# Kernel optimization log

Measured on AMD Instinct MI355X. Metric: run time of the kernel, lower is better.

Reference implementation:

```python
import jax, jax.numpy as jnp
import numpy as np

N_NODES = 100000
N_EDGES = 1600000
N_GRAPHS = 512
NODE_DIM = 64   # len(node_indices)
GRAPH_DIM = 16  # len(graph_indices) == graph_channels
HIDDEN = 128
OUT = 8


def setup_inputs() -> dict:
    key = jax.random.key(0)
    ks = jax.random.split(key, 12)
    x = jax.random.normal(ks[0], (N_NODES, NODE_DIM + GRAPH_DIM), dtype=jnp.float32)
    edge_index = jax.random.randint(ks[1], (2, N_EDGES), 0, N_NODES, dtype=jnp.int64)
    batch = jnp.sort(jax.random.randint(ks[2], (N_NODES,), 0, N_GRAPHS, dtype=jnp.int64))
    def lin(k, fan_in, fan_out):
        lim = 1.0 / np.sqrt(fan_in)
        return jax.random.uniform(k, (fan_in, fan_out), jnp.float32, -lim, lim)
    return {
        "x": x, "edge_index": edge_index, "batch": batch,
        "W1": lin(ks[3], NODE_DIM, HIDDEN), "b1": jnp.zeros((HIDDEN,), jnp.float32),
        "W2": lin(ks[4], HIDDEN, HIDDEN),   "b2": jnp.zeros((HIDDEN,), jnp.float32),
        "Wm1": lin(ks[5], HIDDEN + GRAPH_DIM, HIDDEN), "bm1": jnp.zeros((HIDDEN,), jnp.float32),
        "Wm2": lin(ks[6], HIDDEN, OUT), "bm2": jnp.zeros((OUT,), jnp.float32),
    }


def _gcn_conv(h_in, src, dst, W, b):
    # PyG GCNConv: h = X W; out = D^{-1/2}(A+I)D^{-1/2} h + b, deg over A+I.
    h = h_in @ W                                        # [N, H]
    deg = jnp.zeros((N_NODES,), h.dtype).at[dst].add(1.0) + 1.0  # +1 self loop
    dinv = jax.lax.rsqrt(deg)                           # [N]
    norm = dinv[src] * dinv[dst]                        # [E]
    out = jnp.zeros_like(h).at[dst].add(norm[:, None] * h[src])
    out = out + (dinv * dinv)[:, None] * h              # self-loop term
    return out + b


def _mean_pool(v, batch):
    cnt = jax.ops.segment_sum(jnp.ones((v.shape[0],), v.dtype), batch, num_segments=N_GRAPHS)
    s = jax.ops.segment_sum(v, batch, num_segments=N_GRAPHS)
    return s / jnp.maximum(cnt, 1.0)[:, None]


def reference(x, edge_index, batch, W1, b1, W2, b2, Wm1, bm1, Wm2, bm2):
    src, dst = edge_index[0], edge_index[1]
    node_t = x[:, :NODE_DIM]                 # node_indices slice
    graph_t = _mean_pool(x[:, NODE_DIM:], batch)  # graph_indices slice, pooled [G, 16]
    h = _gcn_conv(node_t, src, dst, W1, b1)
    h = jax.nn.relu(h)                       # dropout is identity in eval mode
    h = _gcn_conv(h, src, dst, W2, b2)
    g = _mean_pool(h, batch)                 # [G, H]
    g = jnp.concatenate([g, graph_t], axis=1)
    g = jax.nn.relu(g @ Wm1 + bm1)
    return g @ Wm2 + bm2                     # [G, OUT]
```

## Files before the change

kernel.cpp:

```cpp
#include <hip/hip_runtime.h>
#include <hip/hip_bf16.h>

#define N_NODES 100000
#define N_EDGES 1600000
#define N_GRAPHS 512
#define NODE_DIM 64
#define GRAPH_DIM 16
#define HIDDEN 128
#define OUT_DIM 8

#define NBUCKETS 391
#define BIN_CAP 8192
#define EPB 4096


__global__ __launch_bounds__(256) void k_binplace(const int* __restrict__ src,
                                                  const int* __restrict__ dst,
                                                  int* __restrict__ gcur,
                                                  unsigned* __restrict__ bin) {
    __shared__ int cnt[NBUCKETS];
    __shared__ int base[NBUCKETS];
    int t = threadIdx.x;
    for (int i = t; i < NBUCKETS; i += 256) cnt[i] = 0;
    __syncthreads();
    int e0 = blockIdx.x * EPB;
#pragma unroll
    for (int k = 0; k < EPB / 256; k++) {
        int e = e0 + k * 256 + t;
        if (e < N_EDGES) atomicAdd(&cnt[dst[e] >> 8], 1);
    }
    __syncthreads();
    for (int i = t; i < NBUCKETS; i += 256) {
        int c = cnt[i];
        base[i] = (c > 0) ? atomicAdd(&gcur[i], c) : 0;
        cnt[i] = 0;
    }
    __syncthreads();
#pragma unroll
    for (int k = 0; k < EPB / 256; k++) {
        int e = e0 + k * 256 + t;
        if (e < N_EDGES) {
            int d = dst[e];
            int b = d >> 8;
            int p = atomicAdd(&cnt[b], 1);
            bin[(size_t)b * BIN_CAP + base[b] + p] = ((unsigned)src[e] << 8) | (unsigned)(d & 255);
        }
    }
}


__global__ __launch_bounds__(256) void k_degBf(const int* __restrict__ gcur,
                                               const unsigned* __restrict__ bin,
                                               int* __restrict__ degcnt,
                                               float* __restrict__ dinv,
                                               int* __restrict__ bsum) {
    __shared__ int cnt[256];
    int b = blockIdx.x, t = threadIdx.x;
    cnt[t] = 0;
    __syncthreads();
    int n = gcur[b];
    const unsigned* seg = bin + (size_t)b * BIN_CAP;
    for (int i = t; i < n; i += 256) atomicAdd(&cnt[seg[i] & 255u], 1);
    __syncthreads();
    int c = cnt[t];
    int node = b * 256 + t;
    if (node < N_NODES) {
        degcnt[node] = c;
        dinv[node] = rsqrtf((float)c + 1.0f);
    }
    __syncthreads();
    for (int o = 128; o > 0; o >>= 1) {
        if (t < o) cnt[t] += cnt[t + o];
        __syncthreads();
    }
    if (t == 0) bsum[b] = cnt[0];
}


__global__ __launch_bounds__(512) void k_scanb(const int* __restrict__ bsum,
                                               int* __restrict__ bofs) {
    __shared__ int s[512];
    int t = threadIdx.x;
    int v = (t < NBUCKETS) ? bsum[t] : 0;
    s[t] = v;
    __syncthreads();
    for (int o = 1; o < 512; o <<= 1) {
        int u = (t >= o) ? s[t - o] : 0;
        __syncthreads();
        s[t] += u;
        __syncthreads();
    }
    if (t < NBUCKETS) bofs[t] = s[t] - v;
}


__global__ __launch_bounds__(256) void k_rowfill(const int* __restrict__ degcnt,
                                                 const int* __restrict__ bofs,
                                                 const int* __restrict__ gcur,
                                                 const unsigned* __restrict__ bin,
                                                 const float* __restrict__ dinv,
                                                 int* __restrict__ row_start,
                                                 int* __restrict__ csr,
                                                 float* __restrict__ csrw) {
    __shared__ int sc[256];
    __shared__ int rsl[256];
    __shared__ int cnt[256];
    __shared__ float dl[256];
    int b = blockIdx.x, t = threadIdx.x;
    int node = b * 256 + t;
    int v = (node < N_NODES) ? degcnt[node] : 0;
    sc[t] = v;
    __syncthreads();
    for (int o = 1; o < 256; o <<= 1) {
        int u = (t >= o) ? sc[t - o] : 0;
        __syncthreads();
        sc[t] += u;
        __syncthreads();
    }
    int rs = bofs[b] + sc[t] - v;
    if (node < N_NODES) row_start[node] = rs;
    rsl[t] = rs;
    cnt[t] = 0;
    dl[t] = rsqrtf((float)v + 1.0f);
    __syncthreads();
    int n = gcur[b];
    const unsigned* seg = bin + (size_t)b * BIN_CAP;
    for (int i = t; i < n; i += 256) {
        unsigned e = seg[i];
        int dlidx = (int)(e & 255u);
        int s = (int)(e >> 8);
        int pos = rsl[dlidx] + atomicAdd(&cnt[dlidx], 1);
        csr[pos] = s;
        csrw[pos] = dinv[s] * dl[dlidx];
    }
}


__global__ __launch_bounds__(256) void k_packstat(const float* __restrict__ x,
                                                  const int* __restrict__ batch,
                                                  ushort* __restrict__ xb,
                                                  float* __restrict__ gt_sum) {
    int t = threadIdx.x;
    int i0 = blockIdx.x * 64;
    for (int idx = t; idx < 64 * 32; idx += 256) {
        int node = i0 + (idx >> 5);
        if (node < N_NODES) {
            int c2 = idx & 31;
            float2 v = *(const float2*)&x[(size_t)node * 80 + c2 * 2];
            __hip_bfloat16 lo = __float2bfloat16(v.x);
            __hip_bfloat16 hi = __float2bfloat16(v.y);
            ushort2 pv = make_ushort2(*(ushort*)&lo, *(ushort*)&hi);
            ((ushort2*)xb)[(size_t)node * 32 + c2] = pv;
        }
    }
    int c = t & 15, sub = t >> 4;
    int iend = min(i0 + 64, N_NODES);
    float acc = 0.0f;
    int g = -1;
    for (int i = i0 + sub; i < iend; i += 16) {
        int bi = batch[i];
        if (bi != g) {
            if (g >= 0) atomicAdd(&gt_sum[g * GRAPH_DIM + c], acc);
            acc = 0.0f; g = bi;
        }
        acc += x[(size_t)i * 80 + NODE_DIM + c];
    }
    if (g >= 0) atomicAdd(&gt_sum[g * GRAPH_DIM + c], acc);
}


#define LDX(s_) __uint_as_float((unsigned)xb[(size_t)(s_)*64 + lane] << 16)

__global__ __launch_bounds__(256) void k_gather1(const int* __restrict__ csr,
                                                 const float* __restrict__ csrw,
                                                 const int* __restrict__ row_start,
                                                 const float* __restrict__ dinv,
                                                 const ushort* __restrict__ xb,
                                                 float* __restrict__ z) {
    int w = threadIdx.x >> 6, lane = threadIdx.x & 63;
    int nA = blockIdx.x * 8 + w * 2;
    int nB = nA + 1;
    int rsA = row_start[nA], reA = (nA == N_NODES - 1) ? N_EDGES : row_start[nA + 1];
    int rsB = row_start[nB], reB = (nB == N_NODES - 1) ? N_EDGES : row_start[nB + 1];
    float aA0 = 0.f, aA1 = 0.f, aA2 = 0.f, aA3 = 0.f;
    float aB0 = 0.f, aB1 = 0.f, aB2 = 0.f, aB3 = 0.f;
    int kA = rsA, kB = rsB;
    while (kA + 4 <= reA && kB + 4 <= reB) {
        int a0 = csr[kA], a1 = csr[kA + 1], a2 = csr[kA + 2], a3 = csr[kA + 3];
        int b0 = csr[kB], b1 = csr[kB + 1], b2 = csr[kB + 2], b3 = csr[kB + 3];
        float wa0 = csrw[kA], wa1 = csrw[kA + 1], wa2 = csrw[kA + 2], wa3 = csrw[kA + 3];
        float wb0 = csrw[kB], wb1 = csrw[kB + 1], wb2 = csrw[kB + 2], wb3 = csrw[kB + 3];
        float vA0 = LDX(a0), vA1 = LDX(a1), vA2 = LDX(a2), vA3 = LDX(a3);
        float vB0 = LDX(b0), vB1 = LDX(b1), vB2 = LDX(b2), vB3 = LDX(b3);
        aA0 += wa0 * vA0; aA1 += wa1 * vA1; aA2 += wa2 * vA2; aA3 += wa3 * vA3;
        aB0 += wb0 * vB0; aB1 += wb1 * vB1; aB2 += wb2 * vB2; aB3 += wb3 * vB3;
        kA += 4; kB += 4;
    }
    while (kA + 4 <= reA) {
        int a0 = csr[kA], a1 = csr[kA + 1], a2 = csr[kA + 2], a3 = csr[kA + 3];
        float wa0 = csrw[kA], wa1 = csrw[kA + 1], wa2 = csrw[kA + 2], wa3 = csrw[kA + 3];
        float vA0 = LDX(a0), vA1 = LDX(a1), vA2 = LDX(a2), vA3 = LDX(a3);
        aA0 += wa0 * vA0; aA1 += wa1 * vA1; aA2 += wa2 * vA2; aA3 += wa3 * vA3;
        kA += 4;
    }
    while (kB + 4 <= reB) {
        int b0 = csr[kB], b1 = csr[kB + 1], b2 = csr[kB + 2], b3 = csr[kB + 3];
        float wb0 = csrw[kB], wb1 = csrw[kB + 1], wb2 = csrw[kB + 2], wb3 = csrw[kB + 3];
        float vB0 = LDX(b0), vB1 = LDX(b1), vB2 = LDX(b2), vB3 = LDX(b3);
        aB0 += wb0 * vB0; aB1 += wb1 * vB1; aB2 += wb2 * vB2; aB3 += wb3 * vB3;
        kB += 4;
    }
    while (kA < reA && kB < reB) {
        int a0 = csr[kA]; int b0 = csr[kB];
        float wa0 = csrw[kA], wb0 = csrw[kB];
        aA0 += wa0 * LDX(a0); aB0 += wb0 * LDX(b0);
        kA++; kB++;
    }
    while (kA < reA) { int a0 = csr[kA]; aA0 += csrw[kA] * LDX(a0); kA++; }
    while (kB < reB) { int b0 = csr[kB]; aB0 += csrw[kB] * LDX(b0); kB++; }
    float dA = dinv[nA], dB = dinv[nB];
    z[(size_t)nA * 64 + lane] = aA0 + aA1 + aA2 + aA3 + dA * dA * LDX(nA);
    z[(size_t)nB * 64 + lane] = aB0 + aB1 + aB2 + aB3 + dB * dB * LDX(nB);
}


__global__ __launch_bounds__(128) void k_gemm64(const float* __restrict__ A,
                                                const float* __restrict__ W,
                                                const float* __restrict__ bias,
                                                ushort* __restrict__ C, int nrows) {
    const int TM = 8, K = 64;
    __shared__ float As[TM][K];
    int row0 = blockIdx.x * TM;
    int j = threadIdx.x;
    for (int idx = threadIdx.x; idx < TM * K; idx += 128) {
        int m = idx / K, k = idx % K;
        int r = row0 + m;
        As[m][k] = (r < nrows) ? A[(size_t)r * K + k] : 0.0f;
    }
    __syncthreads();
    float acc[TM];
#pragma unroll
    for (int m = 0; m < TM; m++) acc[m] = 0.0f;
    for (int k = 0; k < K; k++) {
        float w = W[k * 128 + j];
#pragma unroll
        for (int m = 0; m < TM; m++) acc[m] += As[m][k] * w;
    }
    float b = bias[j];
#pragma unroll
    for (int m = 0; m < TM; m++) {
        int r = row0 + m;
        if (r < nrows) {
            float v = fmaxf(acc[m] + b, 0.0f);
            __hip_bfloat16 hv = __float2bfloat16(v);
            C[(size_t)r * 128 + j] = *(ushort*)&hv;
        }
    }
}


__global__ __launch_bounds__(256) void k_gather2(const int* __restrict__ csr,
                                                 const float* __restrict__ csrw,
                                                 const int* __restrict__ row_start,
                                                 const float* __restrict__ dinv,
                                                 const unsigned* __restrict__ h,
                                                 const int* __restrict__ batch,
                                                 float* __restrict__ gsum2) {
    __shared__ float2 red[8][64];
    int w = threadIdx.x >> 6, lane = threadIdx.x & 63;
    int nA = blockIdx.x * 8 + w * 2;
    int nB = nA + 1;
    int rsA = row_start[nA], reA = (nA == N_NODES - 1) ? N_EDGES : row_start[nA + 1];
    int rsB = row_start[nB], reB = (nB == N_NODES - 1) ? N_EDGES : row_start[nB + 1];
    float2 aA0 = {0.f,0.f}, aA1 = {0.f,0.f}, aA2 = {0.f,0.f}, aA3 = {0.f,0.f};
    float2 aB0 = {0.f,0.f}, aB1 = {0.f,0.f}, aB2 = {0.f,0.f}, aB3 = {0.f,0.f};
    int kA = rsA, kB = rsB;
#define FMA2(acc_, w_, u_) { acc_.x += (w_) * __uint_as_float((u_) << 16); \
                             acc_.y += (w_) * __uint_as_float((u_) & 0xffff0000u); }
    while (kA + 4 <= reA && kB + 4 <= reB) {
        int a0 = csr[kA], a1 = csr[kA + 1], a2 = csr[kA + 2], a3 = csr[kA + 3];
        int b0 = csr[kB], b1 = csr[kB + 1], b2 = csr[kB + 2], b3 = csr[kB + 3];
        float wa0 = csrw[kA], wa1 = csrw[kA + 1], wa2 = csrw[kA + 2], wa3 = csrw[kA + 3];
        float wb0 = csrw[kB], wb1 = csrw[kB + 1], wb2 = csrw[kB + 2], wb3 = csrw[kB + 3];
        unsigned uA0 = h[(size_t)a0 * 64 + lane], uA1 = h[(size_t)a1 * 64 + lane];
        unsigned uA2 = h[(size_t)a2 * 64 + lane], uA3 = h[(size_t)a3 * 64 + lane];
        unsigned uB0 = h[(size_t)b0 * 64 + lane], uB1 = h[(size_t)b1 * 64 + lane];
        unsigned uB2 = h[(size_t)b2 * 64 + lane], uB3 = h[(size_t)b3 * 64 + lane];
        FMA2(aA0, wa0, uA0); FMA2(aA1, wa1, uA1); FMA2(aA2, wa2, uA2); FMA2(aA3, wa3, uA3);
        FMA2(aB0, wb0, uB0); FMA2(aB1, wb1, uB1); FMA2(aB2, wb2, uB2); FMA2(aB3, wb3, uB3);
        kA += 4; kB += 4;
    }
    while (kA + 4 <= reA) {
        int a0 = csr[kA], a1 = csr[kA + 1], a2 = csr[kA + 2], a3 = csr[kA + 3];
        float wa0 = csrw[kA], wa1 = csrw[kA + 1], wa2 = csrw[kA + 2], wa3 = csrw[kA + 3];
        unsigned uA0 = h[(size_t)a0 * 64 + lane], uA1 = h[(size_t)a1 * 64 + lane];
        unsigned uA2 = h[(size_t)a2 * 64 + lane], uA3 = h[(size_t)a3 * 64 + lane];
        FMA2(aA0, wa0, uA0); FMA2(aA1, wa1, uA1); FMA2(aA2, wa2, uA2); FMA2(aA3, wa3, uA3);
        kA += 4;
    }
    while (kB + 4 <= reB) {
        int b0 = csr[kB], b1 = csr[kB + 1], b2 = csr[kB + 2], b3 = csr[kB + 3];
        float wb0 = csrw[kB], wb1 = csrw[kB + 1], wb2 = csrw[kB + 2], wb3 = csrw[kB + 3];
        unsigned uB0 = h[(size_t)b0 * 64 + lane], uB1 = h[(size_t)b1 * 64 + lane];
        unsigned uB2 = h[(size_t)b2 * 64 + lane], uB3 = h[(size_t)b3 * 64 + lane];
        FMA2(aB0, wb0, uB0); FMA2(aB1, wb1, uB1); FMA2(aB2, wb2, uB2); FMA2(aB3, wb3, uB3);
        kB += 4;
    }
    while (kA < reA && kB < reB) {
        int a0 = csr[kA]; int b0 = csr[kB];
        float wa0 = csrw[kA], wb0 = csrw[kB];
        unsigned uA0 = h[(size_t)a0 * 64 + lane], uB0 = h[(size_t)b0 * 64 + lane];
        FMA2(aA0, wa0, uA0); FMA2(aB0, wb0, uB0);
        kA++; kB++;
    }
    while (kA < reA) {
        int a0 = csr[kA]; float wa0 = csrw[kA];
        unsigned uA0 = h[(size_t)a0 * 64 + lane];
        FMA2(aA0, wa0, uA0); kA++;
    }
    while (kB < reB) {
        int b0 = csr[kB]; float wb0 = csrw[kB];
        unsigned uB0 = h[(size_t)b0 * 64 + lane];
        FMA2(aB0, wb0, uB0); kB++;
    }
    float dA = dinv[nA], dB = dinv[nB];
    unsigned usA = h[(size_t)nA * 64 + lane];
    unsigned usB = h[(size_t)nB * 64 + lane];
    float2 rA, rB;
    rA.x = aA0.x + aA1.x + aA2.x + aA3.x + dA * dA * __uint_as_float(usA << 16);
    rA.y = aA0.y + aA1.y + aA2.y + aA3.y + dA * dA * __uint_as_float(usA & 0xffff0000u);
    rB.x = aB0.x + aB1.x + aB2.x + aB3.x + dB * dB * __uint_as_float(usB << 16);
    rB.y = aB0.y + aB1.y + aB2.y + aB3.y + dB * dB * __uint_as_float(usB & 0xffff0000u);
    red[w * 2][lane] = rA;
    red[w * 2 + 1][lane] = rB;
    __syncthreads();
    int g0 = batch[blockIdx.x * 8];
    int g7 = batch[blockIdx.x * 8 + 7];
    if (g0 == g7) {
        if (w == 0) {
            float sx = 0.f, sy = 0.f;
#pragma unroll
            for (int q = 0; q < 8; q++) { sx += red[q][lane].x; sy += red[q][lane].y; }
            atomicAdd(&gsum2[g0 * 128 + 2 * lane], sx);
            atomicAdd(&gsum2[g0 * 128 + 2 * lane + 1], sy);
        }
    } else {
        int gA = batch[nA], gB = batch[nB];
        atomicAdd(&gsum2[gA * 128 + 2 * lane], rA.x);
        atomicAdd(&gsum2[gA * 128 + 2 * lane + 1], rA.y);
        atomicAdd(&gsum2[gB * 128 + 2 * lane], rB.x);
        atomicAdd(&gsum2[gB * 128 + 2 * lane + 1], rB.y);
    }
#undef FMA2
}


__global__ __launch_bounds__(128) void k_mlp(const float* __restrict__ gsum2,
                                             const float* __restrict__ gt_sum,
                                             const int* __restrict__ batch,
                                             const float* __restrict__ W2,
                                             const float* __restrict__ b2,
                                             const float* __restrict__ Wm1,
                                             const float* __restrict__ bm1,
                                             const float* __restrict__ Wm2,
                                             const float* __restrict__ bm2,
                                             float* __restrict__ out) {
    __shared__ float srow[HIDDEN];
    __shared__ float g144[HIDDEN + GRAPH_DIM];
    __shared__ float sm[HIDDEN];
    __shared__ int cnt_sh;
    int b = blockIdx.x;
    int j = threadIdx.x;
    float raw = gsum2[b * 128 + j];
    float gtraw = (j < GRAPH_DIM) ? gt_sum[b * GRAPH_DIM + j] : 0.0f;
    if (j == 0) {
        int lo = 0, hi = N_NODES;
        while (lo < hi) { int m = (lo + hi) >> 1; if (batch[m] < b) lo = m + 1; else hi = m; }
        int a = lo;
        lo = 0; hi = N_NODES;
        while (lo < hi) { int m = (lo + hi) >> 1; if (batch[m] < b + 1) lo = m + 1; else hi = m; }
        cnt_sh = lo - a;
    }
    __syncthreads();
    float inv = 1.0f / fmaxf((float)cnt_sh, 1.0f);
    srow[j] = raw * inv;
    if (j < GRAPH_DIM) g144[128 + j] = gtraw * inv;
    __syncthreads();
    float z = b2[j];
    for (int k = 0; k < 128; k++) z += srow[k] * W2[k * 128 + j];
    g144[j] = z;
    __syncthreads();
    float acc = bm1[j];
    for (int k = 0; k < HIDDEN + GRAPH_DIM; k++) acc += g144[k] * Wm1[k * 128 + j];
    sm[j] = fmaxf(acc, 0.0f);
    __syncthreads();
    if (j < OUT_DIM) {
        float o = bm2[j];
        for (int k = 0; k < 128; k++) o += sm[k] * Wm2[k * OUT_DIM + j];
        out[b * OUT_DIM + j] = o;
    }
}

extern "C" void kernel_launch(void* const* d_in, const int* in_sizes, int n_in,
                              void* d_out, int out_size, void* d_ws, size_t ws_size,
                              hipStream_t stream) {
    const float* x    = (const float*)d_in[0];
    const int*   edge = (const int*)d_in[1];
    const int*   src  = edge;
    const int*   dst  = edge + N_EDGES;
    const int*   batch= (const int*)d_in[2];
    const float* W1   = (const float*)d_in[3];
    const float* b1   = (const float*)d_in[4];
    const float* W2   = (const float*)d_in[5];
    const float* b2   = (const float*)d_in[6];
    const float* Wm1  = (const float*)d_in[7];
    const float* bm1  = (const float*)d_in[8];
    const float* Wm2  = (const float*)d_in[9];
    const float* bm2  = (const float*)d_in[10];
    float* out = (float*)d_out;

    char* ws = (char*)d_ws;
    char* p = ws;
    unsigned* bin   = (unsigned*)p;  p += (size_t)NBUCKETS * BIN_CAP * 4;
    float* A        = (float*)p;     p += (size_t)N_NODES * 64 * 4;
    ushort* h1b     = (ushort*)p;    p += (size_t)N_NODES * 128 * 2;
    ushort* xb      = (ushort*)p;    p += (size_t)N_NODES * 64 * 2;
    int*   csr      = (int*)p;       p += (size_t)N_EDGES * 4;
    float* csrw     = (float*)p;     p += (size_t)N_EDGES * 4;
    int*   degcnt   = (int*)p;       p += (size_t)NBUCKETS * 256 * 4;
    int*   row_start= (int*)p;       p += (size_t)N_NODES * 4;
    float* dinv     = (float*)p;     p += (size_t)N_NODES * 4;
    int*   gcur     = (int*)p;       p += (size_t)NBUCKETS * 4;
    int*   bsum     = (int*)p;       p += 512 * 4;
    int*   bofs     = (int*)p;       p += 512 * 4;
    float* gt_sum   = (float*)p;     p += (size_t)N_GRAPHS * GRAPH_DIM * 4;
    float* gsum2    = (float*)p;     p += (size_t)N_GRAPHS * 128 * 4;

    hipMemsetAsync(gcur,   0, (size_t)NBUCKETS * 4, stream);
    hipMemsetAsync(gt_sum, 0, (size_t)N_GRAPHS * GRAPH_DIM * 4, stream);
    hipMemsetAsync(gsum2,  0, (size_t)N_GRAPHS * 128 * 4, stream);

    k_binplace<<<(N_EDGES + EPB - 1) / EPB, 256, 0, stream>>>(src, dst, gcur, bin);
    k_degBf<<<NBUCKETS, 256, 0, stream>>>(gcur, bin, degcnt, dinv, bsum);
    k_scanb<<<1, 512, 0, stream>>>(bsum, bofs);
    k_rowfill<<<NBUCKETS, 256, 0, stream>>>(degcnt, bofs, gcur, bin, dinv, row_start, csr, csrw);

    k_packstat<<<(N_NODES + 63) / 64, 256, 0, stream>>>(x, batch, xb, gt_sum);

    k_gather1<<<N_NODES / 8, 256, 0, stream>>>(csr, csrw, row_start, dinv, xb, A);
    k_gemm64<<<(N_NODES + 7) / 8, 128, 0, stream>>>(A, W1, b1, h1b, N_NODES);

    k_gather2<<<N_NODES / 8, 256, 0, stream>>>(csr, csrw, row_start, dinv,
                                               (const unsigned*)h1b, batch, gsum2);

    k_mlp<<<N_GRAPHS, 128, 0, stream>>>(gsum2, gt_sum, batch, W2, b2, Wm1, bm1, Wm2, bm2, out);
}
```

Before: 267.9 us.

## Interleave CSR index/weight, use half-wave per node with wider loads, fold memsets

Packs CSR source index and edge weight into one int2 array so each edge needs a single 8-byte load instead of two 4-byte loads. The gather kernels now assign one 32-lane half-wave per node and read wider vectors (two bf16 per lane in gather1, four in gather2), replacing the paired two-node interleaved loops. The zeroing of gt_sum and gsum2 moves from memset calls into earlier kernels (rowfill and gemm64), which removes two launches. The cost is fewer independent node streams per wave, which reduces the memory-level parallelism available to hide gather latency.

```diff
diff --git a/kernel.cpp b/kernel.cpp
--- a/kernel.cpp
+++ b/kernel.cpp
@@ -12,6 +12,9 @@
 #define NBUCKETS 391
 #define BIN_CAP 8192
 #define EPB 4096
+
+__device__ __forceinline__ float bflo(unsigned u) { return __uint_as_float(u << 16); }
+__device__ __forceinline__ float bfhi(unsigned u) { return __uint_as_float(u & 0xffff0000u); }
 
 
 __global__ __launch_bounds__(256) void k_binplace(const int* __restrict__ src,
@@ -100,13 +103,14 @@
                                                  const unsigned* __restrict__ bin,
                                                  const float* __restrict__ dinv,
                                                  int* __restrict__ row_start,
-                                                 int* __restrict__ csr,
-                                                 float* __restrict__ csrw) {
+                                                 int2* __restrict__ csre,
+                                                 float* __restrict__ gt_sum) {
     __shared__ int sc[256];
     __shared__ int rsl[256];
     __shared__ int cnt[256];
     __shared__ float dl[256];
     int b = blockIdx.x, t = threadIdx.x;
+    if (b < 32) gt_sum[b * 256 + t] = 0.0f;
     int node = b * 256 + t;
     int v = (node < N_NODES) ? degcnt[node] : 0;
     sc[t] = v;
@@ -130,8 +134,7 @@
         int dlidx = (int)(e & 255u);
         int s = (int)(e >> 8);
         int pos = rsl[dlidx] + atomicAdd(&cnt[dlidx], 1);
-        csr[pos] = s;
-        csrw[pos] = dinv[s] * dl[dlidx];
+        csre[pos] = make_int2(s, __float_as_int(dinv[s] * dl[dlidx]));
     }
 }
 
@@ -169,67 +172,64 @@
 }
 
 
-#define LDX(s_) __uint_as_float((unsigned)xb[(size_t)(s_)*64 + lane] << 16)
-
-__global__ __launch_bounds__(256) void k_gather1(const int* __restrict__ csr,
-                                                 const float* __restrict__ csrw,
+__global__ __launch_bounds__(256) void k_gather1(const int2* __restrict__ csre,
                                                  const int* __restrict__ row_start,
                                                  const float* __restrict__ dinv,
-                                                 const ushort* __restrict__ xb,
-                                                 float* __restrict__ z) {
-    int w = threadIdx.x >> 6, lane = threadIdx.x & 63;
-    int nA = blockIdx.x * 8 + w * 2;
-    int nB = nA + 1;
-    int rsA = row_start[nA], reA = (nA == N_NODES - 1) ? N_EDGES : row_start[nA + 1];
-    int rsB = row_start[nB], reB = (nB == N_NODES - 1) ? N_EDGES : row_start[nB + 1];
-    float aA0 = 0.f, aA1 = 0.f, aA2 = 0.f, aA3 = 0.f;
-    float aB0 = 0.f, aB1 = 0.f, aB2 = 0.f, aB3 = 0.f;
-    int kA = rsA, kB = rsB;
-    while (kA + 4 <= reA && kB + 4 <= reB) {
-        int a0 = csr[kA], a1 = csr[kA + 1], a2 = csr[kA + 2], a3 = csr[kA + 3];
-        int b0 = csr[kB], b1 = csr[kB + 1], b2 = csr[kB + 2], b3 = csr[kB + 3];
-        float wa0 = csrw[kA], wa1 = csrw[kA + 1], wa2 = csrw[kA + 2], wa3 = csrw[kA + 3];
-        float wb0 = csrw[kB], wb1 = csrw[kB + 1], wb2 = csrw[kB + 2], wb3 = csrw[kB + 3];
-        float vA0 = LDX(a0), vA1 = LDX(a1), vA2 = LDX(a2), vA3 = LDX(a3);
-        float vB0 = LDX(b0), vB1 = LDX(b1), vB2 = LDX(b2), vB3 = LDX(b3);
-        aA0 += wa0 * vA0; aA1 += wa1 * vA1; aA2 += wa2 * vA2; aA3 += wa3 * vA3;
-        aB0 += wb0 * vB0; aB1 += wb1 * vB1; aB2 += wb2 * vB2; aB3 += wb3 * vB3;
-        kA += 4; kB += 4;
-    }
-    while (kA + 4 <= reA) {
-        int a0 = csr[kA], a1 = csr[kA + 1], a2 = csr[kA + 2], a3 = csr[kA + 3];
-        float wa0 = csrw[kA], wa1 = csrw[kA + 1], wa2 = csrw[kA + 2], wa3 = csrw[kA + 3];
-        float vA0 = LDX(a0), vA1 = LDX(a1), vA2 = LDX(a2), vA3 = LDX(a3);
-        aA0 += wa0 * vA0; aA1 += wa1 * vA1; aA2 += wa2 * vA2; aA3 += wa3 * vA3;
-        kA += 4;
-    }
-    while (kB + 4 <= reB) {
-        int b0 = csr[kB], b1 = csr[kB + 1], b2 = csr[kB + 2], b3 = csr[kB + 3];
-        float wb0 = csrw[kB], wb1 = csrw[kB + 1], wb2 = csrw[kB + 2], wb3 = csrw[kB + 3];
-        float vB0 = LDX(b0), vB1 = LDX(b1), vB2 = LDX(b2), vB3 = LDX(b3);
-        aB0 += wb0 * vB0; aB1 += wb1 * vB1; aB2 += wb2 * vB2; aB3 += wb3 * vB3;
-        kB += 4;
-    }
-    while (kA < reA && kB < reB) {
-        int a0 = csr[kA]; int b0 = csr[kB];
-        float wa0 = csrw[kA], wb0 = csrw[kB];
-        aA0 += wa0 * LDX(a0); aB0 += wb0 * LDX(b0);
-        kA++; kB++;
-    }
-    while (kA < reA) { int a0 = csr[kA]; aA0 += csrw[kA] * LDX(a0); kA++; }
-    while (kB < reB) { int b0 = csr[kB]; aB0 += csrw[kB] * LDX(b0); kB++; }
-    float dA = dinv[nA], dB = dinv[nB];
-    z[(size_t)nA * 64 + lane] = aA0 + aA1 + aA2 + aA3 + dA * dA * LDX(nA);
-    z[(size_t)nB * 64 + lane] = aB0 + aB1 + aB2 + aB3 + dB * dB * LDX(nB);
+                                                 const unsigned* __restrict__ xb32,
+                                                 float2* __restrict__ z2) {
+    int w = threadIdx.x >> 6;
+    int half = (threadIdx.x >> 5) & 1;
+    int l = threadIdx.x & 31;
+    int node = blockIdx.x * 8 + w * 2 + half;
+    int rs = row_start[node];
+    int re = (node == N_NODES - 1) ? N_EDGES : row_start[node + 1];
+    float2 a0 = {0.f, 0.f}, a1 = {0.f, 0.f}, a2 = {0.f, 0.f}, a3 = {0.f, 0.f};
+    int k = rs;
+    for (; k + 4 <= re; k += 4) {
+        int2 e0 = csre[k], e1 = csre[k + 1], e2 = csre[k + 2], e3 = csre[k + 3];
+        unsigned u0 = xb32[(size_t)e0.x * 32 + l];
+        unsigned u1 = xb32[(size_t)e1.x * 32 + l];
+        unsigned u2 = xb32[(size_t)e2.x * 32 + l];
+        unsigned u3 = xb32[(size_t)e3.x * 32 + l];
+        float w0 = __int_as_float(e0.y), w1 = __int_as_float(e1.y);
+        float w2 = __int_as_float(e2.y), w3 = __int_as_float(e3.y);
+        a0.x += w0 * bflo(u0); a0.y += w0 * bfhi(u0);
+        a1.x += w1 * bflo(u1); a1.y += w1 * bfhi(u1);
+        a2.x += w2 * bflo(u2); a2.y += w2 * bfhi(u2);
+        a3.x += w3 * bflo(u3); a3.y += w3 * bfhi(u3);
+    }
+    if (k + 2 <= re) {
+        int2 e0 = csre[k], e1 = csre[k + 1];
+        unsigned u0 = xb32[(size_t)e0.x * 32 + l];
+        unsigned u1 = xb32[(size_t)e1.x * 32 + l];
+        float w0 = __int_as_float(e0.y), w1 = __int_as_float(e1.y);
+        a0.x += w0 * bflo(u0); a0.y += w0 * bfhi(u0);
+        a1.x += w1 * bflo(u1); a1.y += w1 * bfhi(u1);
+        k += 2;
+    }
+    if (k < re) {
+        int2 e0 = csre[k];
+        unsigned u0 = xb32[(size_t)e0.x * 32 + l];
+        float w0 = __int_as_float(e0.y);
+        a0.x += w0 * bflo(u0); a0.y += w0 * bfhi(u0);
+    }
+    float d = dinv[node];
+    unsigned us = xb32[(size_t)node * 32 + l];
+    float2 r;
+    r.x = a0.x + a1.x + a2.x + a3.x + d * d * bflo(us);
+    r.y = a0.y + a1.y + a2.y + a3.y + d * d * bfhi(us);
+    z2[(size_t)node * 32 + l] = r;
 }
 
 
 __global__ __launch_bounds__(128) void k_gemm64(const float* __restrict__ A,
                                                 const float* __restrict__ W,
                                                 const float* __restrict__ bias,
-                                                ushort* __restrict__ C, int nrows) {
+                                                ushort* __restrict__ C, int nrows,
+                                                float* __restrict__ gsum2) {
     const int TM = 8, K = 64;
     __shared__ float As[TM][K];
+    if (blockIdx.x < 512) gsum2[blockIdx.x * 128 + threadIdx.x] = 0.0f;
     int row0 = blockIdx.x * TM;
     int j = threadIdx.x;
     for (int idx = threadIdx.x; idx < TM * K; idx += 128) {
@@ -259,99 +259,82 @@
 }
 
 
-__global__ __launch_bounds__(256) void k_gather2(const int* __restrict__ csr,
-                                                 const float* __restrict__ csrw,
+__global__ __launch_bounds__(256) void k_gather2(const int2* __restrict__ csre,
                                                  const int* __restrict__ row_start,
                                                  const float* __restrict__ dinv,
-                                                 const unsigned* __restrict__ h,
+                                                 const uint2* __restrict__ h2,
                                                  const int* __restrict__ batch,
                                                  float* __restrict__ gsum2) {
-    __shared__ float2 red[8][64];
-    int w = threadIdx.x >> 6, lane = threadIdx.x & 63;
-    int nA = blockIdx.x * 8 + w * 2;
-    int nB = nA + 1;
-    int rsA = row_start[nA], reA = (nA == N_NODES - 1) ? N_EDGES : row_start[nA + 1];
-    int rsB = row_start[nB], reB = (nB == N_NODES - 1) ? N_EDGES : row_start[nB + 1];
-    float2 aA0 = {0.f,0.f}, aA1 = {0.f,0.f}, aA2 = {0.f,0.f}, aA3 = {0.f,0.f};
-    float2 aB0 = {0.f,0.f}, aB1 = {0.f,0.f}, aB2 = {0.f,0.f}, aB3 = {0.f,0.f};
-    int kA = rsA, kB = rsB;
-#define FMA2(acc_, w_, u_) { acc_.x += (w_) * __uint_as_float((u_) << 16); \
-                             acc_.y += (w_) * __uint_as_float((u_) & 0xffff0000u); }
-    while (kA + 4 <= reA && kB + 4 <= reB) {
-        int a0 = csr[kA], a1 = csr[kA + 1], a2 = csr[kA + 2], a3 = csr[kA + 3];
-        int b0 = csr[kB], b1 = csr[kB + 1], b2 = csr[kB + 2], b3 = csr[kB + 3];
-        float wa0 = csrw[kA], wa1 = csrw[kA + 1], wa2 = csrw[kA + 2], wa3 = csrw[kA + 3];
-        float wb0 = csrw[kB], wb1 = csrw[kB + 1], wb2 = csrw[kB + 2], wb3 = csrw[kB + 3];
-        unsigned uA0 = h[(size_t)a0 * 64 + lane], uA1 = h[(size_t)a1 * 64 + lane];
-        unsigned uA2 = h[(size_t)a2 * 64 + lane], uA3 = h[(size_t)a3 * 64 + lane];
-        unsigned uB0 = h[(size_t)b0 * 64 + lane], uB1 = h[(size_t)b1 * 64 + lane];
-        unsigned uB2 = h[(size_t)b2 * 64 + lane], uB3 = h[(size_t)b3 * 64 + lane];
-        FMA2(aA0, wa0, uA0); FMA2(aA1, wa1, uA1); FMA2(aA2, wa2, uA2); FMA2(aA3, wa3, uA3);
-        FMA2(aB0, wb0, uB0); FMA2(aB1, wb1, uB1); FMA2(aB2, wb2, uB2); FMA2(aB3, wb3, uB3);
-        kA += 4; kB += 4;
-    }
-    while (kA + 4 <= reA) {
-        int a0 = csr[kA], a1 = csr[kA + 1], a2 = csr[kA + 2], a3 = csr[kA + 3];
-        float wa0 = csrw[kA], wa1 = csrw[kA + 1], wa2 = csrw[kA + 2], wa3 = csrw[kA + 3];
-        unsigned uA0 = h[(size_t)a0 * 64 + lane], uA1 = h[(size_t)a1 * 64 + lane];
-        unsigned uA2 = h[(size_t)a2 * 64 + lane], uA3 = h[(size_t)a3 * 64 + lane];
-        FMA2(aA0, wa0, uA0); FMA2(aA1, wa1, uA1); FMA2(aA2, wa2, uA2); FMA2(aA3, wa3, uA3);
-        kA += 4;
-    }
-    while (kB + 4 <= reB) {
-        int b0 = csr[kB], b1 = csr[kB + 1], b2 = csr[kB + 2], b3 = csr[kB + 3];
-        float wb0 = csrw[kB], wb1 = csrw[kB + 1], wb2 = csrw[kB + 2], wb3 = csrw[kB + 3];
-        unsigned uB0 = h[(size_t)b0 * 64 + lane], uB1 = h[(size_t)b1 * 64 + lane];
-        unsigned uB2 = h[(size_t)b2 * 64 + lane], uB3 = h[(size_t)b3 * 64 + lane];
-        FMA2(aB0, wb0, uB0); FMA2(aB1, wb1, uB1); FMA2(aB2, wb2, uB2); FMA2(aB3, wb3, uB3);
-        kB += 4;
-    }
-    while (kA < reA && kB < reB) {
-        int a0 = csr[kA]; int b0 = csr[kB];
-        float wa0 = csrw[kA], wb0 = csrw[kB];
-        unsigned uA0 = h[(size_t)a0 * 64 + lane], uB0 = h[(size_t)b0 * 64 + lane];
-        FMA2(aA0, wa0, uA0); FMA2(aB0, wb0, uB0);
-        kA++; kB++;
-    }
-    while (kA < reA) {
-        int a0 = csr[kA]; float wa0 = csrw[kA];
-        unsigned uA0 = h[(size_t)a0 * 64 + lane];
-        FMA2(aA0, wa0, uA0); kA++;
-    }
-    while (kB < reB) {
-        int b0 = csr[kB]; float wb0 = csrw[kB];
-        unsigned uB0 = h[(size_t)b0 * 64 + lane];
-        FMA2(aB0, wb0, uB0); kB++;
-    }
-    float dA = dinv[nA], dB = dinv[nB];
-    unsigned usA = h[(size_t)nA * 64 + lane];
-    unsigned usB = h[(size_t)nB * 64 + lane];
-    float2 rA, rB;
-    rA.x = aA0.x + aA1.x + aA2.x + aA3.x + dA * dA * __uint_as_float(usA << 16);
-    rA.y = aA0.y + aA1.y + aA2.y + aA3.y + dA * dA * __uint_as_float(usA & 0xffff0000u);
-    rB.x = aB0.x + aB1.x + aB2.x + aB3.x + dB * dB * __uint_as_float(usB << 16);
-    rB.y = aB0.y + aB1.y + aB2.y + aB3.y + dB * dB * __uint_as_float(usB & 0xffff0000u);
-    red[w * 2][lane] = rA;
-    red[w * 2 + 1][lane] = rB;
-    __syncthreads();
-    int g0 = batch[blockIdx.x * 8];
-    int g7 = batch[blockIdx.x * 8 + 7];
+    __shared__ float4 red[8][32];
+    int w = threadIdx.x >> 6;
+    int half = (threadIdx.x >> 5) & 1;
+    int l = threadIdx.x & 31;
+    int slot = w * 2 + half;
+    int node = blockIdx.x * 8 + slot;
+    int rs = row_start[node];
+    int re = (node == N_NODES - 1) ? N_EDGES : row_start[node + 1];
+    float4 a0 = {0,0,0,0}, a1 = {0,0,0,0}, a2 = {0,0,0,0}, a3 = {0,0,0,0};
+#define FMA4(acc_, w_, u_) { acc_.x += (w_) * bflo((u_).x); acc_.y += (w_) * bfhi((u_).x); \
+                             acc_.z += (w_) * bflo((u_).y); acc_.w += (w_) * bfhi((u_).y); }
+    int k = rs;
+    for (; k + 4 <= re; k += 4) {
+        int2 e0 = csre[k], e1 = csre[k + 1], e2 = csre[k + 2], e3 = csre[k + 3];
+        uint2 u0 = h2[(size_t)e0.x * 32 + l];
+        uint2 u1 = h2[(size_t)e1.x * 32 + l];
+        uint2 u2 = h2[(size_t)e2.x * 32 + l];
+        uint2 u3 = h2[(size_t)e3.x * 32 + l];
+        float w0 = __int_as_float(e0.y), w1 = __int_as_float(e1.y);
+        float w2 = __int_as_float(e2.y), w3 = __int_as_float(e3.y);
+        FMA4(a0, w0, u0); FMA4(a1, w1, u1); FMA4(a2, w2, u2); FMA4(a3, w3, u3);
+    }
+    if (k + 2 <= re) {
+        int2 e0 = csre[k], e1 = csre[k + 1];
+        uint2 u0 = h2[(size_t)e0.x * 32 + l];
+        uint2 u1 = h2[(size_t)e1.x * 32 + l];
+        float w0 = __int_as_float(e0.y), w1 = __int_as_float(e1.y);
+        FMA4(a0, w0, u0); FMA4(a1, w1, u1);
+        k += 2;
+    }
+    if (k < re) {
+        int2 e0 = csre[k];
+        uint2 u0 = h2[(size_t)e0.x * 32 + l];
+        float w0 = __int_as_float(e0.y);
+        FMA4(a0, w0, u0);
+    }
+#undef FMA4
+    float d = dinv[node];
+    float dd = d * d;
+    uint2 us = h2[(size_t)node * 32 + l];
+    float4 r;
+    r.x = a0.x + a1.x + a2.x + a3.x + dd * bflo(us.x);
+    r.y = a0.y + a1.y + a2.y + a3.y + dd * bfhi(us.x);
+    r.z = a0.z + a1.z + a2.z + a3.z + dd * bflo(us.y);
+    r.w = a0.w + a1.w + a2.w + a3.w + dd * bfhi(us.y);
+    red[slot][l] = r;
+    __syncthreads();
+    int base8 = blockIdx.x * 8;
+    int g0 = batch[base8];
+    int g7 = batch[base8 + 7];
     if (g0 == g7) {
-        if (w == 0) {
-            float sx = 0.f, sy = 0.f;
-#pragma unroll
-            for (int q = 0; q < 8; q++) { sx += red[q][lane].x; sy += red[q][lane].y; }
-            atomicAdd(&gsum2[g0 * 128 + 2 * lane], sx);
-            atomicAdd(&gsum2[g0 * 128 + 2 * lane + 1], sy);
+        if (threadIdx.x < 32) {
+            float4 s = {0,0,0,0};
+#pragma unroll
+            for (int q = 0; q < 8; q++) {
+                float4 v = red[q][threadIdx.x];
+                s.x += v.x; s.y += v.y; s.z += v.z; s.w += v.w;
+            }
+            atomicAdd(&gsum2[g0 * 128 + threadIdx.x * 4 + 0], s.x);
+            atomicAdd(&gsum2[g0 * 128 + threadIdx.x * 4 + 1], s.y);
+            atomicAdd(&gsum2[g0 * 128 + threadIdx.x * 4 + 2], s.z);
+            atomicAdd(&gsum2[g0 * 128 + threadIdx.x * 4 + 3], s.w);
         }
     } else {
-        int gA = batch[nA], gB = batch[nB];
-        atomicAdd(&gsum2[gA * 128 + 2 * lane], rA.x);
-        atomicAdd(&gsum2[gA * 128 + 2 * lane + 1], rA.y);
-        atomicAdd(&gsum2[gB * 128 + 2 * lane], rB.x);
-        atomicAdd(&gsum2[gB * 128 + 2 * lane + 1], rB.y);
-    }
-#undef FMA2
+        int g = batch[node];
+        atomicAdd(&gsum2[g * 128 + l * 4 + 0], r.x);
+        atomicAdd(&gsum2[g * 128 + l * 4 + 1], r.y);
+        atomicAdd(&gsum2[g * 128 + l * 4 + 2], r.z);
+        atomicAdd(&gsum2[g * 128 + l * 4 + 3], r.w);
+    }
 }
 
 
@@ -422,11 +405,10 @@
     char* ws = (char*)d_ws;
     char* p = ws;
     unsigned* bin   = (unsigned*)p;  p += (size_t)NBUCKETS * BIN_CAP * 4;
+    int2*  csre     = (int2*)p;      p += (size_t)N_EDGES * 8;
     float* A        = (float*)p;     p += (size_t)N_NODES * 64 * 4;
     ushort* h1b     = (ushort*)p;    p += (size_t)N_NODES * 128 * 2;
     ushort* xb      = (ushort*)p;    p += (size_t)N_NODES * 64 * 2;
-    int*   csr      = (int*)p;       p += (size_t)N_EDGES * 4;
-    float* csrw     = (float*)p;     p += (size_t)N_EDGES * 4;
     int*   degcnt   = (int*)p;       p += (size_t)NBUCKETS * 256 * 4;
     int*   row_start= (int*)p;       p += (size_t)N_NODES * 4;
     float* dinv     = (float*)p;     p += (size_t)N_NODES * 4;
@@ -436,22 +418,20 @@
     float* gt_sum   = (float*)p;     p += (size_t)N_GRAPHS * GRAPH_DIM * 4;
     float* gsum2    = (float*)p;     p += (size_t)N_GRAPHS * 128 * 4;
 
-    hipMemsetAsync(gcur,   0, (size_t)NBUCKETS * 4, stream);
-    hipMemsetAsync(gt_sum, 0, (size_t)N_GRAPHS * GRAPH_DIM * 4, stream);
-    hipMemsetAsync(gsum2,  0, (size_t)N_GRAPHS * 128 * 4, stream);
+    hipMemsetAsync(gcur, 0, (size_t)NBUCKETS * 4, stream);
 
     k_binplace<<<(N_EDGES + EPB - 1) / EPB, 256, 0, stream>>>(src, dst, gcur, bin);
     k_degBf<<<NBUCKETS, 256, 0, stream>>>(gcur, bin, degcnt, dinv, bsum);
     k_scanb<<<1, 512, 0, stream>>>(bsum, bofs);
-    k_rowfill<<<NBUCKETS, 256, 0, stream>>>(degcnt, bofs, gcur, bin, dinv, row_start, csr, csrw);
+    k_rowfill<<<NBUCKETS, 256, 0, stream>>>(degcnt, bofs, gcur, bin, dinv, row_start, csre, gt_sum);
 
     k_packstat<<<(N_NODES + 63) / 64, 256, 0, stream>>>(x, batch, xb, gt_sum);
 
-    k_gather1<<<N_NODES / 8, 256, 0, stream>>>(csr, csrw, row_start, dinv, xb, A);
-    k_gemm64<<<(N_NODES + 7) / 8, 128, 0, stream>>>(A, W1, b1, h1b, N_NODES);
-
-    k_gather2<<<N_NODES / 8, 256, 0, stream>>>(csr, csrw, row_start, dinv,
-                                               (const unsigned*)h1b, batch, gsum2);
+    k_gather1<<<N_NODES / 8, 256, 0, stream>>>(csre, row_start, dinv, (const unsigned*)xb, (float2*)A);
+    k_gemm64<<<(N_NODES + 7) / 8, 128, 0, stream>>>(A, W1, b1, h1b, N_NODES, gsum2);
+
+    k_gather2<<<N_NODES / 8, 256, 0, stream>>>(csre, row_start, dinv,
+                                               (const uint2*)h1b, batch, gsum2);
 
     k_mlp<<<N_GRAPHS, 128, 0, stream>>>(gsum2, gt_sum, batch, W2, b2, Wm1, bm1, Wm2, bm2, out);
 }
```

Result: faster. 258.1 us (-3.7%).
